# Kernel tuning notes

Measured on AMD Instinct MI355X. Metric: run time of the kernel, lower is better.

## Reference

```python
import jax, jax.numpy as jnp
import numpy as np

TOKENS = 4096      # batch*seq flattened
D_IN = 4096        # in_features
D_OUT = 16384      # out_features (4*d_model FFN)


def setup_inputs() -> dict:
    key = jax.random.key(0)
    k1, k2, k3, k4 = jax.random.split(key, 4)
    x = jax.random.normal(k1, (TOKENS, D_IN), dtype=jnp.float32)
    # int8 quantized weight in [-127, 127]
    quantized_weight = jax.random.randint(k2, (D_OUT, D_IN), -127, 128, dtype=jnp.int8)
    # per-output-row scale, positive and small (abs-max / 127 style)
    weight_scale = jax.random.uniform(k3, (D_OUT, 1), dtype=jnp.float32, minval=1e-4, maxval=0.02)
    bias = jax.random.normal(k4, (D_OUT,), dtype=jnp.float32)
    return {"x": x, "quantized_weight": quantized_weight,
            "weight_scale": weight_scale, "bias": bias}


def reference(x, quantized_weight, weight_scale, bias):
    # Dequantize: int8 -> x.dtype, then per-row scale (materializes full weight,
    # exactly as the torch module does).
    w = quantized_weight.astype(x.dtype) * weight_scale  # [D_OUT, D_IN]
    # F.linear: x @ w.T + bias
    return jnp.dot(x, w.T) + bias
```

## Files before the change

kernel.cpp:

```cpp
#include <hip/hip_runtime.h>

#define TOKENS 4096
#define DIN    4096
#define DOUT   16384

#define BM 256
#define BN 256
#define BK 64
#define NT (DIN / BK)

#define X_BYTES ((size_t)TOKENS * DIN * 2)
#define W_BYTES ((size_t)DOUT   * DIN * 2)

typedef __attribute__((ext_vector_type(8))) short short8;
typedef __attribute__((ext_vector_type(4))) float f32x4;

__device__ __forceinline__ unsigned short f2bf(float f) {
    unsigned u = __builtin_bit_cast(unsigned, f);
    u += 0x7fffu + ((u >> 16) & 1u);
    return (unsigned short)(u >> 16);
}

#define GLOAD_LDS16(gptr, lptr)                                                        \
    __builtin_amdgcn_global_load_lds(                                                  \
        (const __attribute__((address_space(1))) unsigned int*)(gptr),                 \
        (__attribute__((address_space(3))) unsigned int*)(lptr), 16, 0, 0)

__global__ __launch_bounds__(256)
void cvt_x_kernel(const float* __restrict__ in, unsigned short* __restrict__ out) {
    const size_t base = ((size_t)blockIdx.x * 256 + threadIdx.x) * 8;
    const float4 a = *(const float4*)&in[base];
    const float4 b = *(const float4*)&in[base + 4];
    uint4 o;
    o.x = (unsigned)f2bf(a.x) | ((unsigned)f2bf(a.y) << 16);
    o.y = (unsigned)f2bf(a.z) | ((unsigned)f2bf(a.w) << 16);
    o.z = (unsigned)f2bf(b.x) | ((unsigned)f2bf(b.y) << 16);
    o.w = (unsigned)f2bf(b.z) | ((unsigned)f2bf(b.w) << 16);
    *(uint4*)&out[base] = o;
}

__global__ __launch_bounds__(256)
void cvt_w_kernel(const int* __restrict__ in, unsigned short* __restrict__ out) {
    const size_t base = ((size_t)blockIdx.x * 256 + threadIdx.x) * 8;
    const int4 a = *(const int4*)&in[base];
    const int4 b = *(const int4*)&in[base + 4];
    uint4 o;
    o.x = (unsigned)f2bf((float)a.x) | ((unsigned)f2bf((float)a.y) << 16);
    o.y = (unsigned)f2bf((float)a.z) | ((unsigned)f2bf((float)a.w) << 16);
    o.z = (unsigned)f2bf((float)b.x) | ((unsigned)f2bf((float)b.y) << 16);
    o.w = (unsigned)f2bf((float)b.z) | ((unsigned)f2bf((float)b.w) << 16);
    *(uint4*)&out[base] = o;
}

__global__ __launch_bounds__(512, 2)
void gemm_bf16_kernel(const unsigned short* __restrict__ xa,
                      const unsigned short* __restrict__ wb,
                      const float* __restrict__ scale,
                      const float* __restrict__ bias,
                      float* __restrict__ out) {
    __shared__ unsigned short smem[2 * 32768];

    const int tid  = threadIdx.x;
    const int lane = tid & 63;
    const int wave = tid >> 6;
    const int wm   = wave >> 2;
    const int wn   = wave & 3;
    const int quad = lane >> 4;
    const int l16  = lane & 15;

    const int nwg = (TOKENS / BM) * (DOUT / BN);
    const int wg  = ((int)blockIdx.x & 7) * (nwg >> 3) + ((int)blockIdx.x >> 3);
    const int m0  = (wg & 15) * BM;
    const int n0  = (wg >> 4) * BN;

    int gAo[2], gBo[2];
#pragma unroll
    for (int i = 0; i < 2; ++i) {
        const int c  = i * 512 + tid;
        const int r  = c >> 3;
        const int gc = (c & 7) ^ (r & 7);
        gAo[i] = (m0 + r) * DIN + gc * 8;
        gBo[i] = (n0 + r) * DIN + gc * 8;
    }

#define STAGE(b, isA, h, kt)                                                             \
    do {                                                                                 \
        const unsigned short* _s = (isA) ? xa : wb;                                      \
        const int _g0 = ((isA) ? gAo[0] : gBo[0]) + (h) * 128 * DIN + (kt) * BK;         \
        const int _g1 = ((isA) ? gAo[1] : gBo[1]) + (h) * 128 * DIN + (kt) * BK;         \
        unsigned short* _d =                                                             \
            &smem[(b) * 32768 + ((isA) ? 0 : 16384) + ((h) * 1024 + wave * 64) * 8];     \
        GLOAD_LDS16(_s + _g0, _d);                                                       \
        GLOAD_LDS16(_s + _g1, _d + 4096);                                                \
    } while (0)

    const int s7    = l16 & 7;
    const int cx0   = (quad ^ s7) * 8;
    const int cx1   = ((quad ^ s7) ^ 4) * 8;
    const int aoff0 = (wm * 128 + l16) * 64 + cx0;
    const int aoff1 = (wm * 128 + l16) * 64 + cx1;
    const int boff0 = (wn * 64 + l16) * 64 + cx0;
    const int boff1 = (wn * 64 + l16) * 64 + cx1;

#define READ_A(mh)                                                                       \
    do {                                                                                 \
        _Pragma("unroll") for (int i = 0; i < 4; ++i) {                                  \
            af[i * 2]     = *(const short8*)&pA[aoff0 + (mh) * 4096 + i * 1024];         \
            af[i * 2 + 1] = *(const short8*)&pA[aoff1 + (mh) * 4096 + i * 1024];         \
        }                                                                                \
    } while (0)

#define READ_B(dst, nh)                                                                  \
    do {                                                                                 \
        _Pragma("unroll") for (int j = 0; j < 2; ++j) {                                  \
            dst[j * 2]     = *(const short8*)&pB[boff0 + (nh) * 2048 + j * 1024];        \
            dst[j * 2 + 1] = *(const short8*)&pB[boff1 + (nh) * 2048 + j * 1024];        \
        }                                                                                \
    } while (0)

#define MFMA_Q(mh, nh, bv)                                                               \
    do {                                                                                 \
        __builtin_amdgcn_s_setprio(1);                                                   \
        _Pragma("unroll") for (int k = 0; k < 2; ++k)                                    \
            _Pragma("unroll") for (int i = 0; i < 4; ++i)                                \
                _Pragma("unroll") for (int j = 0; j < 2; ++j)                            \
                    acc[(mh) * 4 + i][(nh) * 2 + j] =                                    \
                        __builtin_amdgcn_mfma_f32_16x16x32_bf16(                         \
                            af[i * 2 + k], bv[j * 2 + k],                                \
                            acc[(mh) * 4 + i][(nh) * 2 + j], 0, 0, 0);                   \
        __builtin_amdgcn_s_setprio(0);                                                   \
    } while (0)

    STAGE(0, 1, 0, 0);
    STAGE(0, 0, 0, 0);
    STAGE(0, 0, 1, 0);
    STAGE(0, 1, 1, 0);
    STAGE(1, 0, 0, 1);
    STAGE(1, 0, 1, 1);
    STAGE(1, 1, 0, 1);

    f32x4 acc[8][4];
#pragma unroll
    for (int i = 0; i < 8; ++i)
#pragma unroll
        for (int j = 0; j < 4; ++j)
            acc[i][j] = (f32x4){0.f, 0.f, 0.f, 0.f};

    asm volatile("s_waitcnt vmcnt(6)" ::: "memory");
    __builtin_amdgcn_s_barrier();

#pragma unroll 2
    for (int t = 0; t < NT; ++t) {
        const int cur = t & 1;
        const unsigned short* pA = &smem[cur * 32768];
        const unsigned short* pB = pA + 16384;
        short8 af[8], bq0[4], bq1[4];

        READ_A(0);
        READ_B(bq0, 0);
        if (t + 1 < NT) STAGE(cur ^ 1, 1, 1, t + 1);
        MFMA_Q(0, 0, bq0);

        READ_B(bq1, 1);
        MFMA_Q(0, 1, bq1);
        asm volatile("s_waitcnt lgkmcnt(0)" ::: "memory");
        __builtin_amdgcn_s_barrier();

        READ_A(1);
        if (t + 2 < NT) {
            STAGE(cur, 0, 0, t + 2);
            STAGE(cur, 0, 1, t + 2);
        }
        MFMA_Q(1, 1, bq1);
        asm volatile("s_waitcnt lgkmcnt(0)" ::: "memory");
        __builtin_amdgcn_s_barrier();

        if (t + 2 < NT) STAGE(cur, 1, 0, t + 2);
        MFMA_Q(1, 0, bq0);
        if (t < NT - 2) {
            asm volatile("s_waitcnt vmcnt(6)" ::: "memory");
        } else if (t == NT - 2) {
            asm volatile("s_waitcnt vmcnt(0)" ::: "memory");
        }
        __builtin_amdgcn_s_barrier();
    }

#undef STAGE
#undef READ_A
#undef READ_B
#undef MFMA_Q

#pragma unroll
    for (int aj = 0; aj < 4; ++aj) {
        const int col = n0 + wn * 64 + aj * 16 + l16;
        const float s = scale[col];
        const float b = bias[col];
#pragma unroll
        for (int ai = 0; ai < 8; ++ai) {
            const int row0 = m0 + wm * 128 + ai * 16 + quad * 4;
#pragma unroll
            for (int r = 0; r < 4; ++r)
                out[(size_t)(row0 + r) * DOUT + col] = acc[ai][aj][r] * s + b;
        }
    }
}

#define FBM 128
#define FBN 128
#define FBK 32
#define LDSS 40
__global__ __launch_bounds__(256, 2)
void gemm_fallback_kernel(const float* __restrict__ x, const int* __restrict__ qw,
                          const float* __restrict__ scale, const float* __restrict__ bias,
                          float* __restrict__ out) {
    __shared__ unsigned short As[FBM * LDSS];
    __shared__ unsigned short Bs[FBN * LDSS];
    const int tid = threadIdx.x, lane = tid & 63, wave = tid >> 6;
    const int wm = wave >> 1, wn = wave & 1, quad = lane >> 4, l16 = lane & 15;
    const int m0 = blockIdx.x * FBM, n0 = blockIdx.y * FBN;
    const int srow = tid >> 3, scol = (tid & 7) * 4;
    f32x4 acc[4][4];
#pragma unroll
    for (int i = 0; i < 4; ++i)
#pragma unroll
        for (int j = 0; j < 4; ++j) acc[i][j] = (f32x4){0.f, 0.f, 0.f, 0.f};
    for (int k0 = 0; k0 < DIN; k0 += FBK) {
        __syncthreads();
#pragma unroll
        for (int p = 0; p < 4; ++p) {
            const int r = p * 32 + srow;
            const float4 v = *(const float4*)&x[(size_t)(m0 + r) * DIN + k0 + scol];
            const unsigned a01 = (unsigned)f2bf(v.x) | ((unsigned)f2bf(v.y) << 16);
            const unsigned a23 = (unsigned)f2bf(v.z) | ((unsigned)f2bf(v.w) << 16);
            *(unsigned long long*)&As[r * LDSS + scol] =
                (unsigned long long)a01 | ((unsigned long long)a23 << 32);
        }
#pragma unroll
        for (int p = 0; p < 4; ++p) {
            const int r = p * 32 + srow;
            const int4 v = *(const int4*)&qw[(size_t)(n0 + r) * DIN + k0 + scol];
            const unsigned b01 = (unsigned)f2bf((float)v.x) | ((unsigned)f2bf((float)v.y) << 16);
            const unsigned b23 = (unsigned)f2bf((float)v.z) | ((unsigned)f2bf((float)v.w) << 16);
            *(unsigned long long*)&Bs[r * LDSS + scol] =
                (unsigned long long)b01 | ((unsigned long long)b23 << 32);
        }
        __syncthreads();
        short8 af[4], bfv[4];
#pragma unroll
        for (int i = 0; i < 4; ++i)
            af[i] = *(const short8*)&As[(wm * 64 + i * 16 + l16) * LDSS + quad * 8];
#pragma unroll
        for (int j = 0; j < 4; ++j)
            bfv[j] = *(const short8*)&Bs[(wn * 64 + j * 16 + l16) * LDSS + quad * 8];
#pragma unroll
        for (int i = 0; i < 4; ++i)
#pragma unroll
            for (int j = 0; j < 4; ++j)
                acc[i][j] = __builtin_amdgcn_mfma_f32_16x16x32_bf16(af[i], bfv[j], acc[i][j], 0, 0, 0);
    }
#pragma unroll
    for (int j = 0; j < 4; ++j) {
        const int col = n0 + wn * 64 + j * 16 + l16;
        const float s = scale[col], b = bias[col];
#pragma unroll
        for (int i = 0; i < 4; ++i) {
            const int row0 = m0 + wm * 64 + i * 16 + quad * 4;
#pragma unroll
            for (int r = 0; r < 4; ++r)
                out[(size_t)(row0 + r) * DOUT + col] = acc[i][j][r] * s + b;
        }
    }
}

extern "C" void kernel_launch(void* const* d_in, const int* in_sizes, int n_in,
                              void* d_out, int out_size, void* d_ws, size_t ws_size,
                              hipStream_t stream) {
    const float* x     = (const float*)d_in[0];
    const int*   qw    = (const int*)d_in[1];
    const float* scale = (const float*)d_in[2];
    const float* bias  = (const float*)d_in[3];
    float*       out   = (float*)d_out;

    if (ws_size >= X_BYTES + W_BYTES) {
        unsigned short* x_bf = (unsigned short*)d_ws;
        unsigned short* w_bf = (unsigned short*)((char*)d_ws + X_BYTES);
        cvt_x_kernel<<<dim3((TOKENS * DIN) / (256 * 8)), dim3(256), 0, stream>>>(x, x_bf);
        cvt_w_kernel<<<dim3((DOUT * DIN) / (256 * 8)), dim3(256), 0, stream>>>(qw, w_bf);
        gemm_bf16_kernel<<<dim3((TOKENS / BM) * (DOUT / BN)), dim3(512), 0, stream>>>(
            x_bf, w_bf, scale, bias, out);
    } else {
        gemm_fallback_kernel<<<dim3(TOKENS / FBM, DOUT / FBN), dim3(256), 0, stream>>>(
            x, qw, scale, bias, out);
    }
}
```

Baseline: 999.2 us.

## Simplify GEMM main loop to single-barrier prefetch with interleaved LDS reads

Replaces the multi-phase pipeline, which prefetched up to two k-tiles ahead and used three barriers per iteration, with a simpler schedule. Each iteration issues all global-to-LDS loads for the next tile up front, then interleaves finer-grained LDS fragment reads (split per k-half) with MFMA groups, and synchronises once at the end with a full vmcnt/lgkmcnt wait. The aim is fewer barriers and better overlap of LDS reads with MFMAs. The cost is only one tile of prefetch depth, and a full drain of global loads every iteration may expose memory latency.

```diff
diff --git a/kernel.cpp b/kernel.cpp
--- a/kernel.cpp
+++ b/kernel.cpp
@@ -102,42 +102,32 @@
     const int boff0 = (wn * 64 + l16) * 64 + cx0;
     const int boff1 = (wn * 64 + l16) * 64 + cx1;
 
-#define READ_A(mh)                                                                       \
-    do {                                                                                 \
-        _Pragma("unroll") for (int i = 0; i < 4; ++i) {                                  \
-            af[i * 2]     = *(const short8*)&pA[aoff0 + (mh) * 4096 + i * 1024];         \
-            af[i * 2 + 1] = *(const short8*)&pA[aoff1 + (mh) * 4096 + i * 1024];         \
-        }                                                                                \
-    } while (0)
-
-#define READ_B(dst, nh)                                                                  \
-    do {                                                                                 \
-        _Pragma("unroll") for (int j = 0; j < 2; ++j) {                                  \
-            dst[j * 2]     = *(const short8*)&pB[boff0 + (nh) * 2048 + j * 1024];        \
-            dst[j * 2 + 1] = *(const short8*)&pB[boff1 + (nh) * 2048 + j * 1024];        \
-        }                                                                                \
-    } while (0)
-
-#define MFMA_Q(mh, nh, bv)                                                               \
+#define RD_A(dst, kf, mh)                                                                \
+    do {                                                                                 \
+        _Pragma("unroll") for (int i = 0; i < 4; ++i)                                    \
+            dst[i] = *(const short8*)&pA[((kf) ? aoff1 : aoff0) + (mh) * 4096 + i * 1024]; \
+    } while (0)
+
+#define RD_B(dst, kf, nh)                                                                \
+    do {                                                                                 \
+        _Pragma("unroll") for (int j = 0; j < 2; ++j)                                    \
+            dst[j] = *(const short8*)&pB[((kf) ? boff1 : boff0) + (nh) * 2048 + j * 1024]; \
+    } while (0)
+
+#define MM8(aV, bV, mh, nh)                                                              \
     do {                                                                                 \
         __builtin_amdgcn_s_setprio(1);                                                   \
-        _Pragma("unroll") for (int k = 0; k < 2; ++k)                                    \
-            _Pragma("unroll") for (int i = 0; i < 4; ++i)                                \
-                _Pragma("unroll") for (int j = 0; j < 2; ++j)                            \
-                    acc[(mh) * 4 + i][(nh) * 2 + j] =                                    \
-                        __builtin_amdgcn_mfma_f32_16x16x32_bf16(                         \
-                            af[i * 2 + k], bv[j * 2 + k],                                \
-                            acc[(mh) * 4 + i][(nh) * 2 + j], 0, 0, 0);                   \
+        _Pragma("unroll") for (int i = 0; i < 4; ++i)                                    \
+            _Pragma("unroll") for (int j = 0; j < 2; ++j)                                \
+                acc[(mh) * 4 + i][(nh) * 2 + j] = __builtin_amdgcn_mfma_f32_16x16x32_bf16( \
+                    aV[i], bV[j], acc[(mh) * 4 + i][(nh) * 2 + j], 0, 0, 0);             \
         __builtin_amdgcn_s_setprio(0);                                                   \
     } while (0)
 
     STAGE(0, 1, 0, 0);
+    STAGE(0, 1, 1, 0);
     STAGE(0, 0, 0, 0);
     STAGE(0, 0, 1, 0);
-    STAGE(0, 1, 1, 0);
-    STAGE(1, 0, 0, 1);
-    STAGE(1, 0, 1, 1);
-    STAGE(1, 1, 0, 1);
 
     f32x4 acc[8][4];
 #pragma unroll
@@ -146,7 +136,7 @@
         for (int j = 0; j < 4; ++j)
             acc[i][j] = (f32x4){0.f, 0.f, 0.f, 0.f};
 
-    asm volatile("s_waitcnt vmcnt(6)" ::: "memory");
+    asm volatile("s_waitcnt vmcnt(0)" ::: "memory");
     __builtin_amdgcn_s_barrier();
 
 #pragma unroll 2
@@ -154,41 +144,42 @@
         const int cur = t & 1;
         const unsigned short* pA = &smem[cur * 32768];
         const unsigned short* pB = pA + 16384;
-        short8 af[8], bq0[4], bq1[4];
-
-        READ_A(0);
-        READ_B(bq0, 0);
-        if (t + 1 < NT) STAGE(cur ^ 1, 1, 1, t + 1);
-        MFMA_Q(0, 0, bq0);
-
-        READ_B(bq1, 1);
-        MFMA_Q(0, 1, bq1);
-        asm volatile("s_waitcnt lgkmcnt(0)" ::: "memory");
+
+        if (t + 1 < NT) {
+            STAGE(cur ^ 1, 1, 0, t + 1);
+            STAGE(cur ^ 1, 1, 1, t + 1);
+            STAGE(cur ^ 1, 0, 0, t + 1);
+            STAGE(cur ^ 1, 0, 1, t + 1);
+        }
+
+        short8 a0k0[4], a1k0[4], a1k1[4], a0k1[4];
+        short8 b0k0[2], b1k0[2], b0k1[2], b1k1[2];
+
+        RD_A(a0k0, 0, 0);
+        RD_B(b0k0, 0, 0);
+        RD_B(b1k0, 0, 1);
+        MM8(a0k0, b0k0, 0, 0);
+        RD_A(a1k0, 0, 1);
+        MM8(a0k0, b1k0, 0, 1);
+        RD_B(b0k1, 1, 0);
+        MM8(a1k0, b1k0, 1, 1);
+        RD_A(a1k1, 1, 1);
+        MM8(a1k0, b0k0, 1, 0);
+        RD_B(b1k1, 1, 1);
+        MM8(a1k1, b0k1, 1, 0);
+        RD_A(a0k1, 1, 0);
+        MM8(a1k1, b1k1, 1, 1);
+        MM8(a0k1, b1k1, 0, 1);
+        MM8(a0k1, b0k1, 0, 0);
+
+        asm volatile("s_waitcnt vmcnt(0) lgkmcnt(0)" ::: "memory");
         __builtin_amdgcn_s_barrier();
-
-        READ_A(1);
-        if (t + 2 < NT) {
-            STAGE(cur, 0, 0, t + 2);
-            STAGE(cur, 0, 1, t + 2);
-        }
-        MFMA_Q(1, 1, bq1);
-        asm volatile("s_waitcnt lgkmcnt(0)" ::: "memory");
-        __builtin_amdgcn_s_barrier();
-
-        if (t + 2 < NT) STAGE(cur, 1, 0, t + 2);
-        MFMA_Q(1, 0, bq0);
-        if (t < NT - 2) {
-            asm volatile("s_waitcnt vmcnt(6)" ::: "memory");
-        } else if (t == NT - 2) {
-            asm volatile("s_waitcnt vmcnt(0)" ::: "memory");
-        }
-        __builtin_amdgcn_s_barrier();
     }
 
 #undef STAGE
-#undef READ_A
-#undef READ_B
-#undef MFMA_Q
+#undef RD_A
+#undef RD_B
+#undef MM8
 
 #pragma unroll
     for (int aj = 0; aj < 4; ++aj) {
```

After: 970.9 us. 1.03x faster.
